# Kernel tuning notes

Measured on AMD Instinct MI355X. Metric: run time of the kernel, lower is better.

## Reference

```python
import jax, jax.numpy as jnp
import numpy as np

NUM_EMBEDDINGS = 1024
EMBEDDING_DIM = 256


def setup_inputs() -> dict:
    key = jax.random.key(0)
    kx, kw = jax.random.split(key)
    x = jax.random.normal(kx, (64, 32, 32, EMBEDDING_DIM), dtype=jnp.float32)
    # nn.Embedding default init: N(0, 1)
    embedding_weight = jax.random.normal(kw, (NUM_EMBEDDINGS, EMBEDDING_DIM), dtype=jnp.float32)
    return {"x": x, "embedding_weight": embedding_weight}


def reference(x, embedding_weight):
    D = embedding_weight.shape[1]
    x_flat = x.reshape(-1, D)  # [N, D]
    distances = (
        jnp.sum(x_flat * x_flat, axis=1, keepdims=True)
        + jnp.sum(embedding_weight * embedding_weight, axis=1)
        - 2.0 * jnp.matmul(x_flat, embedding_weight.T)
    )
    indices = jnp.argmin(distances, axis=1)  # [N]
    quantized = embedding_weight[indices].reshape(x.shape)
    return quantized, indices
```

## Files before the change

kernel.cpp:

```cpp
#include <hip/hip_runtime.h>


#define K_EMB  1024
#define D_DIM  256
#define N_ROWS 65536

typedef unsigned int u32;
typedef unsigned long long u64;
typedef __attribute__((ext_vector_type(8)))  _Float16 f16x8;
typedef __attribute__((ext_vector_type(4)))  _Float16 f16x4;
typedef __attribute__((ext_vector_type(16))) float    f32x16;

__device__ __forceinline__ u32 f32_sortable(float f) {
    u32 u = __float_as_uint(f);
    return u ^ ((u32)((int)u >> 31) | 0x80000000u);
}
__device__ __forceinline__ float f32_unsort(u32 u) {
    u32 v = (u & 0x80000000u) ? (u ^ 0x80000000u) : ~u;
    return __uint_as_float(v);
}

#define GLDS(gp, lp) __builtin_amdgcn_global_load_lds( \
    (const __attribute__((address_space(1))) void*)(gp), \
    (__attribute__((address_space(3))) void*)(lp), 16, 0, 0)

__global__ void vq_prep(const float* __restrict__ emb,
                        _Float16* __restrict__ ehi,
                        _Float16* __restrict__ cn2,
                        float* __restrict__ cnormf) {
    int gid = blockIdx.x * 256 + threadIdx.x;
    int code = gid >> 6, lane = gid & 63;
    float4 v = ((const float4*)(emb + (size_t)code * D_DIM))[lane];
    f16x4 hv = {(_Float16)v.x, (_Float16)v.y, (_Float16)v.z, (_Float16)v.w};
    ((f16x4*)(ehi + (size_t)code * D_DIM))[lane] = hv;
    float s = v.x * v.x + v.y * v.y + v.z * v.z + v.w * v.w;
    #pragma unroll
    for (int off = 32; off > 0; off >>= 1) s += __shfl_down(s, off, 64);
    if (lane == 0) {
        float cn = 0.5f * s;
        cnormf[code] = cn;
        _Float16 ch = (_Float16)cn;
        _Float16 cl = (_Float16)(cn - (float)ch);
        f16x8 e = {};
        e[0] = (_Float16)(-(float)ch);
        e[1] = (_Float16)(-(float)cl);
        ((f16x8*)cn2)[code] = e;
    }
}

__global__ __launch_bounds__(512, 4) void vq_main(
    const float* __restrict__ x, const float* __restrict__ emb,
    const _Float16* __restrict__ eh, const _Float16* __restrict__ cn2,
    const float* __restrict__ cnormf,
    float* __restrict__ outq, float* __restrict__ outi)
{
    __shared__ _Float16 T[2][2][8192];
    __shared__ u32 xchg[2][128][3];
    __shared__ int winners[128];

    const int t = threadIdx.x, w = t >> 6, lane = t & 63;
    const int m = lane & 31, kh = lane >> 5;
    const int p = w >> 1;
    const int h = w & 1;
    const int blkrow = blockIdx.x * 128;
    const int kh4 = kh * 4;

    auto stage = [&](int c) {
        _Float16* dstb = &T[c & 1][h][0];
        const _Float16* srcb = eh + (size_t)(h * 512 + c * 32 + m) * D_DIM + kh * 8;
        #pragma unroll
        for (int i = 0; i < 4; i++) {
            int r = p * 4 + i;
            GLDS(srcb + r * 16, dstb + r * 512);
        }
    };

    stage(0);

    f16x8 bh[16];
    {
        char* xb = (char*)&T[1][0][0];
        #pragma unroll
        for (int k = 0; k < 2; k++) {
            #pragma unroll
            for (int i = 0; i < 8; i++) {
                int row = i * 8 + w;
                float4 v = *(const float4*)(
                    x + (size_t)(blkrow + k * 64 + row) * D_DIM + lane * 4);
                f16x4 hv = {(_Float16)v.x, (_Float16)v.y,
                            (_Float16)v.z, (_Float16)v.w};
                u32 byte = (u32)(row * 512 + lane * 8) ^ ((u32)(row & 7) << 4);
                *(f16x4*)(xb + byte) = hv;
            }
            __syncthreads();
            if ((p >> 1) == k) {
                int lr = (p & 1) * 32 + m;
                #pragma unroll
                for (int s = 0; s < 16; s++) {
                    u32 byte = (u32)(lr * 512 + s * 32 + kh * 16)
                             ^ ((u32)(lr & 7) << 4);
                    bh[s] = *(const f16x8*)(xb + byte);
                }
            }
            __syncthreads();
        }
    }
    f16x8 xe = {};
    if (kh == 0) { xe[0] = (_Float16)1.0f; xe[1] = (_Float16)1.0f; }

    u32 A1 = 0, A2 = 0, A3 = 0;

    auto t3 = [](u32& c1, u32& c2, u32& c3, u32 pv) {
        u32 u2 = c1 < pv ? c1 : pv;
        u32 u3 = c2 < pv ? c2 : pv;
        c1 = c1 > pv ? c1 : pv;
        c2 = u2 > c2 ? u2 : c2;
        c3 = u3 > c3 ? u3 : c3;
    };

    for (int c = 0; c < 16; ++c) {
        __syncthreads();
        if (c + 1 < 16) stage(c + 1);
        const f16x8* Af = (const f16x8*)&T[c & 1][h][0];
        f16x8 e = ((const f16x8*)cn2)[h * 512 + c * 32 + m];
        f32x16 a = {};
        #pragma unroll
        for (int s = 0; s < 16; s++) {
            f16x8 fa = Af[(2 * s + kh) * 32 + m];
            a = __builtin_amdgcn_mfma_f32_32x32x16_f16(fa, bh[s], a, 0, 0, 0);
        }
        a = __builtin_amdgcn_mfma_f32_32x32x16_f16(e, xe, a, 0, 0, 0);
        const u32 sbase = (u32)(h * 512 + c * 32) + kh4;
        #pragma unroll
        for (int r = 0; r < 16; r++) {
            u32 code = sbase + (r & 3) + 8 * (r >> 2);
            u32 pk = (f32_sortable(a[r]) & 0xFFFFFC00u) | code;
            t3(A1, A2, A3, pk);
        }
    }

    {
        u32 q1 = (u32)__shfl_xor((int)A1, 32, 64);
        u32 q2 = (u32)__shfl_xor((int)A2, 32, 64);
        u32 q3 = (u32)__shfl_xor((int)A3, 32, 64);
        t3(A1, A2, A3, q1); t3(A1, A2, A3, q2); t3(A1, A2, A3, q3);
    }

    if (kh == 0) {
        int ra = p * 32 + m;
        xchg[h][ra][0] = A1; xchg[h][ra][1] = A2; xchg[h][ra][2] = A3;
    }
    __syncthreads();

    const int lr = w * 16 + (lane & 15);
    u32 c1 = 0, c2 = 0, c3 = 0;
    #pragma unroll
    for (int hh = 0; hh < 2; hh++) {
        t3(c1, c2, c3, xchg[hh][lr][0]);
        t3(c1, c2, c3, xchg[hh][lr][1]);
        t3(c1, c2, c3, xchg[hh][lr][2]);
    }

    float s1f = f32_unsort(c1), s2f = f32_unsort(c2), s3f = f32_unsort(c3);
    u32 i1 = c1 & 1023u, i2 = c2 & 1023u, i3 = c3 & 1023u;
    const bool act = lane < 16;
    bool need = (s1f - s2f) <= 0.25f;
    if (act && !need) winners[lr] = (int)i1;
    u64 mask = __ballot(act && need);
    while (mask) {
        int r = __ffsll((unsigned long long)mask) - 1;
        mask &= mask - 1;
        int row = blkrow + w * 16 + r;
        u32 d1 = (u32)__shfl((int)i1, r, 64);
        u32 d2 = (u32)__shfl((int)i2, r, 64);
        u32 d3 = (u32)__shfl((int)i3, r, 64);
        float g3 = __shfl(s1f - s3f, r, 64);
        int ncand = (g3 <= 0.25f) ? 3 : 2;
        float4 xv = ((const float4*)(x + (size_t)row * D_DIM))[lane];
        float bs = -3.0e38f; int bi = 0x7fffffff;
        u32 cand[3] = {d1, d2, d3};
        for (int q = 0; q < ncand; q++) {
            int ccd = (int)cand[q];
            float4 ev = ((const float4*)(emb + (size_t)ccd * D_DIM))[lane];
            float d = xv.x * ev.x + xv.y * ev.y + xv.z * ev.z + xv.w * ev.w;
            #pragma unroll
            for (int dd = 1; dd < 64; dd <<= 1) d += __shfl_xor(d, dd, 64);
            float sc = d - cnormf[ccd];
            if (sc > bs || (sc == bs && ccd < bi)) { bs = sc; bi = ccd; }
        }
        if (lane == 0) winners[w * 16 + r] = bi;
    }

    if (act) outi[blkrow + lr] = (float)winners[lr];
    #pragma unroll 8
    for (int r = 0; r < 16; r++) {
        int idx = winners[w * 16 + r];
        int row = blkrow + w * 16 + r;
        float4 qv = ((const float4*)(emb + (size_t)idx * D_DIM))[lane];
        ((float4*)(outq + (size_t)row * D_DIM))[lane] = qv;
    }
}

extern "C" void kernel_launch(void* const* d_in, const int* in_sizes, int n_in,
                              void* d_out, int out_size, void* d_ws, size_t ws_size,
                              hipStream_t stream) {
    const float* x   = (const float*)d_in[0];
    const float* emb = (const float*)d_in[1];
    float* outq = (float*)d_out;
    float* outi = outq + (size_t)N_ROWS * D_DIM;

    _Float16* ehi = (_Float16*)d_ws;
    _Float16* cn2 = ehi + (size_t)K_EMB * D_DIM;
    float* cnormf = (float*)(cn2 + (size_t)K_EMB * 8);

    vq_prep<<<K_EMB / 4, 256, 0, stream>>>(emb, ehi, cn2, cnormf);
    vq_main<<<N_ROWS / 128, 512, 0, stream>>>(x, emb, ehi, cn2, cnormf,
                                              outq, outi);
}
```

Measured before the change: 156.9 us.

## Load pre-swizzled codebook fragments directly into registers instead of LDS staging

The prep kernel now writes the fp16 codebook in an MFMA-fragment-ordered layout, so each lane of the main kernel can read its A operands with coalesced 16-byte global loads straight into registers. These loads are double-buffered in registers across the K loop. This removes the LDS double buffer, the global_load_lds staging and the per-chunk __syncthreads. Blocks shrink to 256 threads and 64 rows, using less LDS and allowing more blocks per CU. In exchange, every wave now re-reads the codebook from L2/global memory with no sharing through LDS, and register pressure rises from the fragment buffers.

```diff
diff --git a/kernel.cpp b/kernel.cpp
--- a/kernel.cpp
+++ b/kernel.cpp
@@ -20,19 +20,21 @@
     return __uint_as_float(v);
 }
 
-#define GLDS(gp, lp) __builtin_amdgcn_global_load_lds( \
-    (const __attribute__((address_space(1))) void*)(gp), \
-    (__attribute__((address_space(3))) void*)(lp), 16, 0, 0)
-
 __global__ void vq_prep(const float* __restrict__ emb,
-                        _Float16* __restrict__ ehi,
+                        _Float16* __restrict__ ehp,
                         _Float16* __restrict__ cn2,
                         float* __restrict__ cnormf) {
     int gid = blockIdx.x * 256 + threadIdx.x;
     int code = gid >> 6, lane = gid & 63;
     float4 v = ((const float4*)(emb + (size_t)code * D_DIM))[lane];
     f16x4 hv = {(_Float16)v.x, (_Float16)v.y, (_Float16)v.z, (_Float16)v.w};
-    ((f16x4*)(ehi + (size_t)code * D_DIM))[lane] = hv;
+    {
+        int h = code >> 9, c = (code >> 5) & 15, m = code & 31;
+        int s = lane >> 2, kh = (lane >> 1) & 1, jlo = lane & 1;
+        size_t halfs = ((((size_t)(h * 16 + c) * 16 + s) * 64) + kh * 32 + m) * 8
+                     + jlo * 4;
+        *(f16x4*)(ehp + halfs) = hv;
+    }
     float s = v.x * v.x + v.y * v.y + v.z * v.z + v.w * v.w;
     #pragma unroll
     for (int off = 32; off > 0; off >>= 1) s += __shfl_down(s, off, 64);
@@ -48,61 +50,43 @@
     }
 }
 
-__global__ __launch_bounds__(512, 4) void vq_main(
+__global__ __launch_bounds__(256, 4) void vq_main(
     const float* __restrict__ x, const float* __restrict__ emb,
-    const _Float16* __restrict__ eh, const _Float16* __restrict__ cn2,
+    const _Float16* __restrict__ ehp, const _Float16* __restrict__ cn2,
     const float* __restrict__ cnormf,
     float* __restrict__ outq, float* __restrict__ outi)
 {
-    __shared__ _Float16 T[2][2][8192];
-    __shared__ u32 xchg[2][128][3];
-    __shared__ int winners[128];
+    __shared__ _Float16 XS[16384];
+    __shared__ u32 xchg[2][64][3];
+    __shared__ int winners[64];
 
     const int t = threadIdx.x, w = t >> 6, lane = t & 63;
     const int m = lane & 31, kh = lane >> 5;
     const int p = w >> 1;
     const int h = w & 1;
-    const int blkrow = blockIdx.x * 128;
+    const int blkrow = blockIdx.x * 64;
     const int kh4 = kh * 4;
-
-    auto stage = [&](int c) {
-        _Float16* dstb = &T[c & 1][h][0];
-        const _Float16* srcb = eh + (size_t)(h * 512 + c * 32 + m) * D_DIM + kh * 8;
-        #pragma unroll
-        for (int i = 0; i < 4; i++) {
-            int r = p * 4 + i;
-            GLDS(srcb + r * 16, dstb + r * 512);
-        }
-    };
-
-    stage(0);
 
     f16x8 bh[16];
     {
-        char* xb = (char*)&T[1][0][0];
+        char* xb = (char*)XS;
         #pragma unroll
-        for (int k = 0; k < 2; k++) {
-            #pragma unroll
-            for (int i = 0; i < 8; i++) {
-                int row = i * 8 + w;
-                float4 v = *(const float4*)(
-                    x + (size_t)(blkrow + k * 64 + row) * D_DIM + lane * 4);
-                f16x4 hv = {(_Float16)v.x, (_Float16)v.y,
-                            (_Float16)v.z, (_Float16)v.w};
-                u32 byte = (u32)(row * 512 + lane * 8) ^ ((u32)(row & 7) << 4);
-                *(f16x4*)(xb + byte) = hv;
-            }
-            __syncthreads();
-            if ((p >> 1) == k) {
-                int lr = (p & 1) * 32 + m;
-                #pragma unroll
-                for (int s = 0; s < 16; s++) {
-                    u32 byte = (u32)(lr * 512 + s * 32 + kh * 16)
-                             ^ ((u32)(lr & 7) << 4);
-                    bh[s] = *(const f16x8*)(xb + byte);
-                }
-            }
-            __syncthreads();
+        for (int i = 0; i < 16; i++) {
+            int row = i * 4 + w;
+            float4 v = *(const float4*)(
+                x + (size_t)(blkrow + row) * D_DIM + lane * 4);
+            f16x4 hv = {(_Float16)v.x, (_Float16)v.y,
+                        (_Float16)v.z, (_Float16)v.w};
+            u32 byte = (u32)(row * 512 + lane * 8) ^ ((u32)(row & 7) << 4);
+            *(f16x4*)(xb + byte) = hv;
+        }
+        __syncthreads();
+        int lr = p * 32 + m;
+        #pragma unroll
+        for (int s = 0; s < 16; s++) {
+            u32 byte = (u32)(lr * 512 + s * 32 + kh * 16)
+                     ^ ((u32)(lr & 7) << 4);
+            bh[s] = *(const f16x8*)(xb + byte);
         }
     }
     f16x8 xe = {};
@@ -118,17 +102,32 @@
         c3 = u3 > c3 ? u3 : c3;
     };
 
+    const char* pc = (const char*)ehp + ((size_t)h * 16384 + lane) * 16;
+    const f16x8* cn2f = (const f16x8*)cn2 + (size_t)h * 512 + m;
+
+    f16x8 f0[4], f1[4];
+    #define LD4(B) { (B)[0] = *(const f16x8*)(pc); \
+                     (B)[1] = *(const f16x8*)(pc + 1024); \
+                     (B)[2] = *(const f16x8*)(pc + 2048); \
+                     (B)[3] = *(const f16x8*)(pc + 3072); pc += 4096; }
+    #define MF4(B, S) { \
+        a = __builtin_amdgcn_mfma_f32_32x32x16_f16((B)[0], bh[(S)],     a, 0, 0, 0); \
+        a = __builtin_amdgcn_mfma_f32_32x32x16_f16((B)[1], bh[(S) + 1], a, 0, 0, 0); \
+        a = __builtin_amdgcn_mfma_f32_32x32x16_f16((B)[2], bh[(S) + 2], a, 0, 0, 0); \
+        a = __builtin_amdgcn_mfma_f32_32x32x16_f16((B)[3], bh[(S) + 3], a, 0, 0, 0); }
+
+    LD4(f0);
     for (int c = 0; c < 16; ++c) {
-        __syncthreads();
-        if (c + 1 < 16) stage(c + 1);
-        const f16x8* Af = (const f16x8*)&T[c & 1][h][0];
-        f16x8 e = ((const f16x8*)cn2)[h * 512 + c * 32 + m];
         f32x16 a = {};
-        #pragma unroll
-        for (int s = 0; s < 16; s++) {
-            f16x8 fa = Af[(2 * s + kh) * 32 + m];
-            a = __builtin_amdgcn_mfma_f32_32x32x16_f16(fa, bh[s], a, 0, 0, 0);
-        }
+        f16x8 e = cn2f[c * 32];
+        LD4(f1);
+        MF4(f0, 0);
+        LD4(f0);
+        MF4(f1, 4);
+        LD4(f1);
+        MF4(f0, 8);
+        LD4(f0);
+        MF4(f1, 12);
         a = __builtin_amdgcn_mfma_f32_32x32x16_f16(e, xe, a, 0, 0, 0);
         const u32 sbase = (u32)(h * 512 + c * 32) + kh4;
         #pragma unroll
@@ -138,6 +137,8 @@
             t3(A1, A2, A3, pk);
         }
     }
+    #undef LD4
+    #undef MF4
 
     {
         u32 q1 = (u32)__shfl_xor((int)A1, 32, 64);
@@ -209,11 +210,11 @@
     float* outq = (float*)d_out;
     float* outi = outq + (size_t)N_ROWS * D_DIM;
 
-    _Float16* ehi = (_Float16*)d_ws;
-    _Float16* cn2 = ehi + (size_t)K_EMB * D_DIM;
+    _Float16* ehp = (_Float16*)d_ws;
+    _Float16* cn2 = ehp + (size_t)K_EMB * D_DIM;
     float* cnormf = (float*)(cn2 + (size_t)K_EMB * 8);
 
-    vq_prep<<<K_EMB / 4, 256, 0, stream>>>(emb, ehi, cn2, cnormf);
-    vq_main<<<N_ROWS / 128, 512, 0, stream>>>(x, emb, ehi, cn2, cnormf,
-                                              outq, outi);
-}
+    vq_prep<<<K_EMB / 4, 256, 0, stream>>>(emb, ehp, cn2, cnormf);
+    vq_main<<<N_ROWS / 64, 256, 0, stream>>>(x, emb, ehp, cn2, cnormf,
+                                             outq, outi);
+}
```

Measured after the change: 180.0 us. +14.7%, slower.

## Pack code norms into LDS and hand-schedule barriers with partial vmcnt waits

Applied to the files above, without the earlier changes.

Code norms are packed as two halves in one u32, loaded once per block into shared memory, and rebuilt into the MFMA operand from LDS instead of being fetched per chunk from global memory. The main loop replaces __syncthreads with explicit s_barrier plus s_waitcnt vmcnt(4), so the previous chunk's async LDS loads are waited on while the next chunk's loads stay in flight. MFMA sections are wrapped in s_setprio to favour the matrix work. The hand-written waitcnt depends on the compiler's exact count of outstanding loads. The CNs fill reaches the first read only through the vmcnt wait and barrier, not through an explicit sync.

```diff
diff --git a/kernel.cpp b/kernel.cpp
--- a/kernel.cpp
+++ b/kernel.cpp
@@ -26,7 +26,7 @@
 
 __global__ void vq_prep(const float* __restrict__ emb,
                         _Float16* __restrict__ ehi,
-                        _Float16* __restrict__ cn2,
+                        u32* __restrict__ cn2c,
                         float* __restrict__ cnormf) {
     int gid = blockIdx.x * 256 + threadIdx.x;
     int code = gid >> 6, lane = gid & 63;
@@ -41,20 +41,21 @@
         cnormf[code] = cn;
         _Float16 ch = (_Float16)cn;
         _Float16 cl = (_Float16)(cn - (float)ch);
-        f16x8 e = {};
-        e[0] = (_Float16)(-(float)ch);
-        e[1] = (_Float16)(-(float)cl);
-        ((f16x8*)cn2)[code] = e;
+        union { _Float16 hh[2]; u32 uu; } pk;
+        pk.hh[0] = (_Float16)(-(float)ch);
+        pk.hh[1] = (_Float16)(-(float)cl);
+        cn2c[code] = pk.uu;
     }
 }
 
 __global__ __launch_bounds__(512, 4) void vq_main(
     const float* __restrict__ x, const float* __restrict__ emb,
-    const _Float16* __restrict__ eh, const _Float16* __restrict__ cn2,
+    const _Float16* __restrict__ eh, const u32* __restrict__ cn2c,
     const float* __restrict__ cnormf,
     float* __restrict__ outq, float* __restrict__ outi)
 {
     __shared__ _Float16 T[2][2][8192];
+    __shared__ u32 CNs[1024];
     __shared__ u32 xchg[2][128][3];
     __shared__ int winners[128];
 
@@ -76,6 +77,9 @@
     };
 
     stage(0);
+
+    CNs[t] = cn2c[t];
+    CNs[t + 512] = cn2c[t + 512];
 
     f16x8 bh[16];
     {
@@ -119,17 +123,32 @@
     };
 
     for (int c = 0; c < 16; ++c) {
-        __syncthreads();
-        if (c + 1 < 16) stage(c + 1);
+        __builtin_amdgcn_sched_barrier(0);
+        __builtin_amdgcn_s_barrier();
+        if (c < 15) {
+            stage(c + 1);
+            asm volatile("s_waitcnt vmcnt(4)" ::: "memory");
+        } else {
+            asm volatile("s_waitcnt vmcnt(0)" ::: "memory");
+        }
+        __builtin_amdgcn_sched_barrier(0);
+        __builtin_amdgcn_s_barrier();
+
         const f16x8* Af = (const f16x8*)&T[c & 1][h][0];
-        f16x8 e = ((const f16x8*)cn2)[h * 512 + c * 32 + m];
+        union { u32 uu; _Float16 hh[2]; } uv;
+        uv.uu = CNs[h * 512 + c * 32 + m];
+        f16x8 e = {};
+        e[0] = uv.hh[0]; e[1] = uv.hh[1];
         f32x16 a = {};
+        __builtin_amdgcn_s_setprio(1);
         #pragma unroll
         for (int s = 0; s < 16; s++) {
             f16x8 fa = Af[(2 * s + kh) * 32 + m];
             a = __builtin_amdgcn_mfma_f32_32x32x16_f16(fa, bh[s], a, 0, 0, 0);
         }
         a = __builtin_amdgcn_mfma_f32_32x32x16_f16(e, xe, a, 0, 0, 0);
+        __builtin_amdgcn_s_setprio(0);
+
         const u32 sbase = (u32)(h * 512 + c * 32) + kh4;
         #pragma unroll
         for (int r = 0; r < 16; r++) {
@@ -210,10 +229,10 @@
     float* outi = outq + (size_t)N_ROWS * D_DIM;
 
     _Float16* ehi = (_Float16*)d_ws;
-    _Float16* cn2 = ehi + (size_t)K_EMB * D_DIM;
-    float* cnormf = (float*)(cn2 + (size_t)K_EMB * 8);
-
-    vq_prep<<<K_EMB / 4, 256, 0, stream>>>(emb, ehi, cn2, cnormf);
-    vq_main<<<N_ROWS / 128, 512, 0, stream>>>(x, emb, ehi, cn2, cnormf,
+    u32* cn2c = (u32*)(ehi + (size_t)K_EMB * D_DIM);
+    float* cnormf = (float*)(cn2c + K_EMB);
+
+    vq_prep<<<K_EMB / 4, 256, 0, stream>>>(emb, ehi, cn2c, cnormf);
+    vq_main<<<N_ROWS / 128, 512, 0, stream>>>(x, emb, ehi, cn2c, cnormf,
                                               outq, outi);
 }
```

Measured after the change: 155.1 us. About the same (-1.1%).
